# Kernel tuning notes

Hardware: AMD Instinct MI355X
Metric: run time of the kernel (lower is better)

## Reference

```python
import jax, jax.numpy as jnp
import numpy as np

N_NODES = 100000
N_EDGES = 1600000
B_GRAPHS = 64
F_IN = 128
HID = 128
N_CLS = 16
EPS = 1e-5


def setup_inputs() -> dict:
    key = jax.random.key(0)
    ks = jax.random.split(key, 12)
    x = jax.random.normal(ks[0], (N_NODES, F_IN), jnp.float32)
    edge_index = jax.random.randint(ks[1], (2, N_EDGES), 0, N_NODES, dtype=jnp.int32)
    batch = jnp.sort(jax.random.randint(ks[2], (N_NODES,), 0, B_GRAPHS, dtype=jnp.int32))
    sc = lambda fi: 1.0 / np.sqrt(fi)
    return {
        'x': x, 'edge_index': edge_index, 'batch': batch,
        'W1': jax.random.normal(ks[3], (F_IN, HID), jnp.float32) * sc(F_IN),
        'b1': jnp.zeros((HID,), jnp.float32),
        'g1': jnp.ones((HID,), jnp.float32), 'be1': jnp.zeros((HID,), jnp.float32),
        'W2': jax.random.normal(ks[4], (HID, HID), jnp.float32) * sc(HID),
        'b2': jnp.zeros((HID,), jnp.float32),
        'g2': jnp.ones((HID,), jnp.float32), 'be2': jnp.zeros((HID,), jnp.float32),
        'Wg1': jax.random.normal(ks[5], (HID, HID // 2), jnp.float32) * sc(HID),
        'bg1': jnp.zeros((HID // 2,), jnp.float32),
        'Wg2': jax.random.normal(ks[6], (HID // 2, 1), jnp.float32) * sc(HID // 2),
        'bg2': jnp.zeros((1,), jnp.float32),
        'Wc': jax.random.normal(ks[7], (HID, N_CLS), jnp.float32) * sc(HID),
        'bc': jnp.zeros((N_CLS,), jnp.float32),
    }


def gcn_conv(x, src, dst, W, b):
    # GCNConv: h = D^{-1/2}(A+I)D^{-1/2} (x W) + b, self-loops added
    n = x.shape[0]
    h = x @ W
    loop = jnp.arange(n, dtype=src.dtype)
    s = jnp.concatenate([src, loop])
    d = jnp.concatenate([dst, loop])
    deg = jax.ops.segment_sum(jnp.ones_like(d, dtype=h.dtype), d, num_segments=n)
    dinv = jax.lax.rsqrt(deg)  # deg >= 1 thanks to self-loops
    norm = dinv[s] * dinv[d]           # [E+N]
    msg = h[s] * norm[:, None]         # [E+N, HID] gather-transform
    return jax.ops.segment_sum(msg, d, num_segments=n) + b  # scatter-add


def layernorm(x, g, be):
    mu = jnp.mean(x, axis=-1, keepdims=True)
    var = jnp.mean(jnp.square(x - mu), axis=-1, keepdims=True)
    return (x - mu) * jax.lax.rsqrt(var + EPS) * g + be


def att_pool(x, batch, Wg1, bg1, Wg2, bg2, n_graphs):
    gate = jax.nn.relu(x @ Wg1 + bg1) @ Wg2 + bg2           # [N,1]
    gmax = jax.ops.segment_max(gate, batch, num_segments=n_graphs)
    e = jnp.exp(gate - gmax[batch])
    denom = jax.ops.segment_sum(e, batch, num_segments=n_graphs)
    alpha = e / denom[batch]                                 # segment softmax
    return jax.ops.segment_sum(alpha * x, batch, num_segments=n_graphs)


def reference(x, edge_index, batch, W1, b1, g1, be1, W2, b2, g2, be2,
              Wg1, bg1, Wg2, bg2, Wc, bc):
    src, dst = edge_index[0], edge_index[1]
    h = gcn_conv(x, src, dst, W1, b1)
    h = jax.nn.relu(layernorm(h, g1, be1))  # dropout is identity at eval
    h = gcn_conv(h, src, dst, W2, b2)
    h = jax.nn.relu(layernorm(h, g2, be2))
    pooled = att_pool(h, batch, Wg1, bg1, Wg2, bg2, B_GRAPHS)  # [B, HID]
    return pooled @ Wc + bc  # [B, N_CLS]
```

## Files before the change

kernel.cpp:

```cpp
#include <hip/hip_runtime.h>


typedef unsigned short ushort_t;
typedef unsigned int uint_t;
typedef __attribute__((ext_vector_type(8))) short short8;
typedef __attribute__((ext_vector_type(4))) float floatx4;

#define POOL_S 16
#define PAD_DEG 64

__device__ inline ushort_t bf16_rn(float f) {
  uint_t u = __float_as_uint(f);
  u += 0x7fffu + ((u >> 16) & 1u);
  return (ushort_t)(u >> 16);
}
__device__ inline float bf16_lo(uint_t v) { return __uint_as_float(v << 16); }
__device__ inline float bf16_hi(uint_t v) { return __uint_as_float(v & 0xffff0000u); }
__device__ inline uint_t bf16_pack(float a, float b) {
  return (uint_t)bf16_rn(a) | ((uint_t)bf16_rn(b) << 16);
}

__global__ __launch_bounds__(256) void prep_weights_kernel(
    const float* __restrict__ W1, const float* __restrict__ W2,
    const float* __restrict__ Wg1, ushort_t* __restrict__ Wt) {
  int id = blockIdx.x * 256 + threadIdx.x;
  float v;
  if (id < 16384) {
    int n = id >> 7, k = id & 127;
    v = W1[k * 128 + n];
  } else if (id < 32768) {
    int i2 = id - 16384;
    int n = i2 >> 7, k = i2 & 127;
    v = W2[k * 128 + n];
  } else {
    int i2 = id - 32768;
    int n = i2 >> 7, k = i2 & 127;
    v = Wg1[k * 64 + n];
  }
  Wt[id] = bf16_rn(v);
}

template <int TM, int NC, bool IN_F32, bool SCALE, bool BIASRELU, bool GATEDOT>
__device__ __forceinline__ void gemm_tile(
    const void* __restrict__ in, const ushort_t* __restrict__ Wt,
    const float* __restrict__ bias, const float* __restrict__ dinv,
    ushort_t* __restrict__ out, int M, int row0,
    const float* __restrict__ Wg2, const float* __restrict__ bg2,
    float* __restrict__ gate_out, short* As) {
  constexpr int CT = NC / 16;
  constexpr int RT = TM / 64;
  const int t = threadIdx.x;
#pragma unroll
  for (int i = 0; i < TM / 16; ++i) {
    int chunk = t + i * 256;
    int rr = chunk >> 4, c8 = (chunk & 15) * 8;
    int row = row0 + rr;
    short8 val = {0, 0, 0, 0, 0, 0, 0, 0};
    if (IN_F32) {
      const float* inf = (const float*)in;
      if (row < M) {
        float4 v0 = *(const float4*)(inf + (size_t)row * 128 + c8);
        float4 v1 = *(const float4*)(inf + (size_t)row * 128 + c8 + 4);
        val[0] = (short)bf16_rn(v0.x); val[1] = (short)bf16_rn(v0.y);
        val[2] = (short)bf16_rn(v0.z); val[3] = (short)bf16_rn(v0.w);
        val[4] = (short)bf16_rn(v1.x); val[5] = (short)bf16_rn(v1.y);
        val[6] = (short)bf16_rn(v1.z); val[7] = (short)bf16_rn(v1.w);
      }
    } else {
      const short* inb = (const short*)in;
      if (row < M) val = *(const short8*)(inb + (size_t)row * 128 + c8);
    }
    *(short8*)&As[rr * 136 + c8] = val;
  }
  __syncthreads();

  const int wave = t >> 6, lane = t & 63;
  const int m16 = lane & 15, quad = lane >> 4;
  floatx4 acc[RT][CT];
#pragma unroll
  for (int rt = 0; rt < RT; ++rt)
#pragma unroll
    for (int ct = 0; ct < CT; ++ct) acc[rt][ct] = (floatx4){0.f, 0.f, 0.f, 0.f};
#pragma unroll
  for (int ks = 0; ks < 4; ++ks) {
    int koff = ks * 32 + quad * 8;
    short8 a[RT];
#pragma unroll
    for (int rt = 0; rt < RT; ++rt)
      a[rt] = *(const short8*)&As[(wave * 16 + rt * 64 + m16) * 136 + koff];
#pragma unroll
    for (int ct = 0; ct < CT; ++ct) {
      short8 b = *(const short8*)((const short*)Wt + (size_t)(ct * 16 + m16) * 128 + koff);
#pragma unroll
      for (int rt = 0; rt < RT; ++rt)
        acc[rt][ct] = __builtin_amdgcn_mfma_f32_16x16x32_bf16(a[rt], b, acc[rt][ct], 0, 0, 0);
    }
  }

  float bv[CT];
  if (BIASRELU) {
#pragma unroll
    for (int ct = 0; ct < CT; ++ct) bv[ct] = bias[ct * 16 + m16];
  }

  if (GATEDOT) {
    float w2[CT];
#pragma unroll
    for (int ct = 0; ct < CT; ++ct) w2[ct] = Wg2[ct * 16 + m16];
    float bg2v = bg2[0];
#pragma unroll
    for (int rt = 0; rt < RT; ++rt) {
#pragma unroll
      for (int reg = 0; reg < 4; ++reg) {
        float p = 0.f;
#pragma unroll
        for (int ct = 0; ct < CT; ++ct)
          p += fmaxf(acc[rt][ct][reg] + bv[ct], 0.f) * w2[ct];
        p += __shfl_xor(p, 1);
        p += __shfl_xor(p, 2);
        p += __shfl_xor(p, 4);
        p += __shfl_xor(p, 8);
        if (m16 == 0) {
          int row = row0 + wave * 16 + rt * 64 + quad * 4 + reg;
          if (row < M) gate_out[row] = p + bg2v;
        }
      }
    }
    return;
  }

#pragma unroll
  for (int rt = 0; rt < RT; ++rt) {
#pragma unroll
    for (int reg = 0; reg < 4; ++reg) {
      int row = row0 + wave * 16 + rt * 64 + quad * 4 + reg;
      if (row < M) {
        float mult = SCALE ? dinv[row] : 1.f;
#pragma unroll
        for (int ct = 0; ct < CT; ++ct) {
          float v = acc[rt][ct][reg];
          if (BIASRELU) v = fmaxf(v + bv[ct], 0.f);
          else if (SCALE) v *= mult;
          out[(size_t)row * NC + ct * 16 + m16] = bf16_rn(v);
        }
      }
    }
  }
}

__global__ __launch_bounds__(256) void place_gemm1_kernel(
    const int* __restrict__ src, const int* __restrict__ dst,
    int* __restrict__ fill, int* __restrict__ srcs_pad, int E,
    const float* __restrict__ x, const ushort_t* __restrict__ Wt,
    ushort_t* __restrict__ hs, int M, int nPlace, int nGemm) {
  __shared__ short As[64 * 136];
  int b = blockIdx.x;
  int gi = b / 5, rem = b - gi * 5;
  if (rem == 4) {
    if (gi < nGemm)
      gemm_tile<64, 128, true, false, false, false>(
          x, Wt, nullptr, nullptr, hs, M, gi * 64, nullptr, nullptr, nullptr, As);
    return;
  }
  int pi = gi * 4 + rem;
  if (pi < nPlace) {
    int e = pi * 256 + threadIdx.x;
    if (e < E) {
      int d = dst[e];
      int pos = atomicAdd(&fill[d], 1);
      if (pos < PAD_DEG) srcs_pad[(size_t)d * PAD_DEG + pos] = src[e];
    }
  }
}

__global__ __launch_bounds__(256) void scale_dinv_kernel(
    uint4* __restrict__ hs4, const int* __restrict__ fill,
    float* __restrict__ dinv, int* __restrict__ srcs_pad,
    int Nnodes, int nU4) {
  int id = blockIdx.x * 256 + threadIdx.x;
  if (id >= nU4) return;
  int row = id >> 4;
  float dv = rsqrtf((float)(fill[row] + 1));
  uint4 v = hs4[id];
  uint4 o;
  o.x = bf16_pack(bf16_lo(v.x) * dv, bf16_hi(v.x) * dv);
  o.y = bf16_pack(bf16_lo(v.y) * dv, bf16_hi(v.y) * dv);
  o.z = bf16_pack(bf16_lo(v.z) * dv, bf16_hi(v.z) * dv);
  o.w = bf16_pack(bf16_lo(v.w) * dv, bf16_hi(v.w) * dv);
  hs4[id] = o;
  if ((id & 15) == 0) {
    dinv[row] = dv;
    int cnt = fill[row];
    if (cnt > PAD_DEG) cnt = PAD_DEG;
    int K = (cnt + 3) & ~3;
    for (int p = cnt; p < K; ++p) srcs_pad[(size_t)row * PAD_DEG + p] = Nnodes;
  }
}

template <int NC, bool SCALE, bool BIASRELU, bool GATEDOT>
__global__ __launch_bounds__(256) void gemm_mfma_kernel(
    const ushort_t* __restrict__ in, const ushort_t* __restrict__ Wt,
    const float* __restrict__ bias, const float* __restrict__ dinv,
    ushort_t* __restrict__ out, int M,
    const float* __restrict__ Wg2, const float* __restrict__ bg2,
    float* __restrict__ gate_out) {
  __shared__ short As[128 * 136];
  gemm_tile<128, NC, false, SCALE, BIASRELU, GATEDOT>(
      in, Wt, bias, dinv, out, M, blockIdx.x * 128, Wg2, bg2, gate_out, As);
}

__device__ __forceinline__ void add8(float* a, uint4 v) {
  a[0] += bf16_lo(v.x); a[1] += bf16_hi(v.x);
  a[2] += bf16_lo(v.y); a[3] += bf16_hi(v.y);
  a[4] += bf16_lo(v.z); a[5] += bf16_hi(v.z);
  a[6] += bf16_lo(v.w); a[7] += bf16_hi(v.w);
}

__global__ __launch_bounds__(256) void aggregate_ln_kernel(
    const ushort_t* __restrict__ hs, const int* __restrict__ fill,
    const int* __restrict__ srcs_pad, const float* __restrict__ dinv,
    const float* __restrict__ bias, const float* __restrict__ gamma,
    const float* __restrict__ beta, ushort_t* __restrict__ out, int N) {
  int n = (blockIdx.x * 256 + threadIdx.x) >> 6;
  int lane = threadIdx.x & 63;
  if (n >= N) return;
  const int col = lane & 15, epar = lane >> 4;
  const uint4* hs4 = (const uint4*)hs;
  int sreg = srcs_pad[(size_t)n * PAD_DEG + lane];
  int count = fill[n];
  if (count > PAD_DEG) count = PAD_DEG;
  const int K = (count + 3) & ~3;
  float a[8] = {0.f, 0.f, 0.f, 0.f, 0.f, 0.f, 0.f, 0.f};
  int i = epar;
  for (; i + 12 < K; i += 16) {
    int s0 = __shfl(sreg, i);
    int s1 = __shfl(sreg, i + 4);
    int s2 = __shfl(sreg, i + 8);
    int s3 = __shfl(sreg, i + 12);
    uint4 v0 = hs4[(size_t)s0 * 16 + col];
    uint4 v1 = hs4[(size_t)s1 * 16 + col];
    uint4 v2 = hs4[(size_t)s2 * 16 + col];
    uint4 v3 = hs4[(size_t)s3 * 16 + col];
    add8(a, v0); add8(a, v1); add8(a, v2); add8(a, v3);
  }
  for (; i < K; i += 4) {
    int s = __shfl(sreg, i);
    uint4 v = hs4[(size_t)s * 16 + col];
    add8(a, v);
  }
#pragma unroll
  for (int k = 0; k < 8; ++k) {
    a[k] += __shfl_xor(a[k], 16);
    a[k] += __shfl_xor(a[k], 32);
  }
  {
    uint4 sv = hs4[(size_t)n * 16 + col];
    add8(a, sv);
  }
  float dv = dinv[n];
  float4 b0 = *(const float4*)(bias + 8 * col);
  float4 b1 = *(const float4*)(bias + 8 * col + 4);
  float y[8];
  y[0] = a[0] * dv + b0.x; y[1] = a[1] * dv + b0.y;
  y[2] = a[2] * dv + b0.z; y[3] = a[3] * dv + b0.w;
  y[4] = a[4] * dv + b1.x; y[5] = a[5] * dv + b1.y;
  y[6] = a[6] * dv + b1.z; y[7] = a[7] * dv + b1.w;
  float s1 = 0.f, s2 = 0.f;
#pragma unroll
  for (int k = 0; k < 8; ++k) { s1 += y[k]; s2 += y[k] * y[k]; }
#pragma unroll
  for (int off = 1; off <= 8; off <<= 1) {
    s1 += __shfl_xor(s1, off);
    s2 += __shfl_xor(s2, off);
  }
  float mu = s1 * (1.f / 128.f);
  float var = s2 * (1.f / 128.f) - mu * mu;
  float rinv = rsqrtf(var + 1e-5f);
  float4 g0 = *(const float4*)(gamma + 8 * col);
  float4 g1 = *(const float4*)(gamma + 8 * col + 4);
  float4 e0 = *(const float4*)(beta + 8 * col);
  float4 e1 = *(const float4*)(beta + 8 * col + 4);
  float o[8];
  o[0] = fmaxf((y[0] - mu) * rinv * g0.x + e0.x, 0.f);
  o[1] = fmaxf((y[1] - mu) * rinv * g0.y + e0.y, 0.f);
  o[2] = fmaxf((y[2] - mu) * rinv * g0.z + e0.z, 0.f);
  o[3] = fmaxf((y[3] - mu) * rinv * g0.w + e0.w, 0.f);
  o[4] = fmaxf((y[4] - mu) * rinv * g1.x + e1.x, 0.f);
  o[5] = fmaxf((y[5] - mu) * rinv * g1.y + e1.y, 0.f);
  o[6] = fmaxf((y[6] - mu) * rinv * g1.z + e1.z, 0.f);
  o[7] = fmaxf((y[7] - mu) * rinv * g1.w + e1.w, 0.f);
  if (epar == 0) {
    uint4 pk;
    pk.x = bf16_pack(o[0], o[1]); pk.y = bf16_pack(o[2], o[3]);
    pk.z = bf16_pack(o[4], o[5]); pk.w = bf16_pack(o[6], o[7]);
    ((uint4*)out)[(size_t)n * 16 + col] = pk;
  }
}

__device__ inline int lower_bound_i(const int* a, int n, int key) {
  int lo = 0, hi = n;
  while (lo < hi) {
    int mid = (lo + hi) >> 1;
    if (a[mid] < key) lo = mid + 1; else hi = mid;
  }
  return lo;
}

__global__ __launch_bounds__(256) void gate_stats_kernel(
    const float* __restrict__ gate, const int* __restrict__ batch,
    float* __restrict__ gmax_out, float* __restrict__ ginv_out, int N) {
  int g = blockIdx.x, t = threadIdx.x;
  __shared__ float red[256];
  __shared__ float s_gmax;
  int lo = lower_bound_i(batch, N, g);
  int hi = lower_bound_i(batch, N, g + 1);
  float m = -3.4e38f;
  for (int i = lo + t; i < hi; i += 256) m = fmaxf(m, gate[i]);
  red[t] = m;
  __syncthreads();
  for (int off = 128; off; off >>= 1) {
    if (t < off) red[t] = fmaxf(red[t], red[t + off]);
    __syncthreads();
  }
  if (t == 0) s_gmax = red[0];
  __syncthreads();
  float gmax = s_gmax;
  __syncthreads();
  float ssum = 0.f;
  for (int i = lo + t; i < hi; i += 256) ssum += expf(gate[i] - gmax);
  red[t] = ssum;
  __syncthreads();
  for (int off = 128; off; off >>= 1) {
    if (t < off) red[t] += red[t + off];
    __syncthreads();
  }
  if (t == 0) {
    gmax_out[g] = gmax;
    ginv_out[g] = red[0] > 0.f ? 1.f / red[0] : 0.f;
  }
}

__global__ __launch_bounds__(256) void pool_partial_kernel(
    const ushort_t* __restrict__ h2, const float* __restrict__ gate,
    const int* __restrict__ batch, const float* __restrict__ gmax_in,
    float* __restrict__ partial, int N) {
  int g = blockIdx.x / POOL_S, sub = blockIdx.x % POOL_S;
  int t = threadIdx.x;
  __shared__ float redx[256];
  __shared__ float redy[256];
  int lo = lower_bound_i(batch, N, g);
  int hi = lower_bound_i(batch, N, g + 1);
  int len = hi - lo;
  int chunk = (len + POOL_S - 1) / POOL_S;
  int a = lo + sub * chunk;
  int b = a + chunk < hi ? a + chunk : hi;
  float gmax = gmax_in[g];
  int p = t & 63, strm = t >> 6;
  const uint_t* h2u = (const uint_t*)h2;
  float accx = 0.f, accy = 0.f;
  int i = a + strm;
  for (; i + 8 <= b; i += 8) {
    float e0 = expf(gate[i] - gmax);
    float e1 = expf(gate[i + 4] - gmax);
    uint_t v0 = h2u[(size_t)i * 64 + p];
    uint_t v1 = h2u[(size_t)(i + 4) * 64 + p];
    accx += e0 * bf16_lo(v0) + e1 * bf16_lo(v1);
    accy += e0 * bf16_hi(v0) + e1 * bf16_hi(v1);
  }
  for (; i < b; i += 4) {
    float e = expf(gate[i] - gmax);
    uint_t v = h2u[(size_t)i * 64 + p];
    accx += e * bf16_lo(v);
    accy += e * bf16_hi(v);
  }
  redx[t] = accx;
  redy[t] = accy;
  __syncthreads();
  if (t < 64) {
    float px = redx[t] + redx[t + 64] + redx[t + 128] + redx[t + 192];
    float py = redy[t] + redy[t + 64] + redy[t + 128] + redy[t + 192];
    float* dstp = partial + (size_t)blockIdx.x * 128;
    dstp[2 * t] = px;
    dstp[2 * t + 1] = py;
  }
}

__global__ __launch_bounds__(128) void classify_kernel(
    const float* __restrict__ partial, const float* __restrict__ ginv,
    const float* __restrict__ Wc, const float* __restrict__ bc,
    float* __restrict__ out) {
  int g = blockIdx.x, t = threadIdx.x;
  __shared__ float pooled[128];
  float s = 0.f;
#pragma unroll
  for (int k = 0; k < POOL_S; ++k)
    s += partial[((size_t)g * POOL_S + k) * 128 + t];
  pooled[t] = s * ginv[g];
  __syncthreads();
  if (t < 16) {
    float o = bc[t];
    for (int ff = 0; ff < 128; ++ff) o = fmaf(pooled[ff], Wc[ff * 16 + t], o);
    out[g * 16 + t] = o;
  }
}

extern "C" void kernel_launch(void* const* d_in, const int* in_sizes, int n_in,
                              void* d_out, int out_size, void* d_ws, size_t ws_size,
                              hipStream_t stream) {
  const float* x   = (const float*)d_in[0];
  const int*   ei  = (const int*)d_in[1];
  const int*   bat = (const int*)d_in[2];
  const float* W1  = (const float*)d_in[3];
  const float* b1  = (const float*)d_in[4];
  const float* g1  = (const float*)d_in[5];
  const float* be1 = (const float*)d_in[6];
  const float* W2  = (const float*)d_in[7];
  const float* b2  = (const float*)d_in[8];
  const float* g2  = (const float*)d_in[9];
  const float* be2 = (const float*)d_in[10];
  const float* Wg1 = (const float*)d_in[11];
  const float* bg1 = (const float*)d_in[12];
  const float* Wg2 = (const float*)d_in[13];
  const float* bg2 = (const float*)d_in[14];
  const float* Wc  = (const float*)d_in[15];
  const float* bc  = (const float*)d_in[16];

  const int N = in_sizes[0] / 128;
  const int E = in_sizes[1] / 2;
  const int B = out_size / 16;
  const int* src = ei;
  const int* dst = ei + E;

  const int Np = (N + 3) & ~3;

  int* fill      = (int*)d_ws;
  float* dinv    = (float*)(fill + Np);
  float* gatep   = dinv + Np;
  float* gmax    = gatep + Np;
  float* ginv    = gmax + B;
  float* ppart   = ginv + B;
  int* srcs_pad  = (int*)(ppart + (size_t)B * POOL_S * 128);
  ushort_t* Wt   = (ushort_t*)(srcs_pad + (size_t)N * PAD_DEG);
  ushort_t* hs   = Wt + 40960;
  ushort_t* h1   = hs + (size_t)128 * (N + 1);

  hipMemsetAsync(fill, 0, sizeof(int) * (size_t)Np, stream);
  hipMemsetAsync(hs + (size_t)128 * N, 0, 256, stream);

  const int Pb = (E + 255) / 256;
  const int Gb64 = (N + 63) / 64;
  const int Gg128 = (N + 127) / 128;
  const int nU4 = N * 16;

  prep_weights_kernel<<<160, 256, 0, stream>>>(W1, W2, Wg1, Wt);

  int nGroups = (Pb + 3) / 4;
  if (Gb64 > nGroups) nGroups = Gb64;
  place_gemm1_kernel<<<5 * nGroups, 256, 0, stream>>>(
      src, dst, fill, srcs_pad, E, x, Wt, hs, N, Pb, Gb64);

  scale_dinv_kernel<<<(nU4 + 255) / 256, 256, 0, stream>>>(
      (uint4*)hs, fill, dinv, srcs_pad, N, nU4);

  aggregate_ln_kernel<<<(N + 3) / 4, 256, 0, stream>>>(
      hs, fill, srcs_pad, dinv, b1, g1, be1, h1, N);
  gemm_mfma_kernel<128, true, false, false><<<Gg128, 256, 0, stream>>>(
      h1, Wt + 16384, nullptr, dinv, hs, N, nullptr, nullptr, nullptr);
  aggregate_ln_kernel<<<(N + 3) / 4, 256, 0, stream>>>(
      hs, fill, srcs_pad, dinv, b2, g2, be2, h1, N);
  gemm_mfma_kernel<64, false, true, true><<<Gg128, 256, 0, stream>>>(
      h1, Wt + 32768, bg1, nullptr, nullptr, N, Wg2, bg2, gatep);

  gate_stats_kernel<<<B, 256, 0, stream>>>(gatep, bat, gmax, ginv, N);
  pool_partial_kernel<<<B * POOL_S, 256, 0, stream>>>(h1, gatep, bat, gmax, ppart, N);
  classify_kernel<<<B, 128, 0, stream>>>(ppart, ginv, Wc, bc, (float*)d_out);
}
```

Before: 414.5 us.

## Vectorize edge placement 8-per-thread and fuse gate stats into pooling via online softmax

The edge-placement part of the fused place/GEMM1 kernel now has each thread load 8 src/dst pairs with int4 loads and issue 8 independent atomics. The block interleave changes from 4 place blocks per GEMM block to 1 place block per 2 GEMM blocks. The separate gate_stats kernel is removed: each pool block computes a local max and exp-sum over its chunk, and classify_kernel merges the partials with a rescaled (online) softmax. This saves one launch and one pass over the gate array, at the cost of redundant reductions inside each pool block and more atomics in flight per thread.

Result: slower. 426.9 us (+3.0%).

```diff
diff --git a/kernel.cpp b/kernel.cpp
--- a/kernel.cpp
+++ b/kernel.cpp
@@ -155,20 +155,46 @@
     ushort_t* __restrict__ hs, int M, int nPlace, int nGemm) {
   __shared__ short As[64 * 136];
   int b = blockIdx.x;
-  int gi = b / 5, rem = b - gi * 5;
-  if (rem == 4) {
-    if (gi < nGemm)
+  int gi = b / 3, rem = b - gi * 3;
+  if (rem < 2) {
+    int g = gi * 2 + rem;
+    if (g < nGemm)
       gemm_tile<64, 128, true, false, false, false>(
-          x, Wt, nullptr, nullptr, hs, M, gi * 64, nullptr, nullptr, nullptr, As);
+          x, Wt, nullptr, nullptr, hs, M, g * 64, nullptr, nullptr, nullptr, As);
     return;
   }
-  int pi = gi * 4 + rem;
-  if (pi < nPlace) {
-    int e = pi * 256 + threadIdx.x;
-    if (e < E) {
-      int d = dst[e];
-      int pos = atomicAdd(&fill[d], 1);
-      if (pos < PAD_DEG) srcs_pad[(size_t)d * PAD_DEG + pos] = src[e];
+  if (gi < nPlace) {
+    int e0 = (gi * 256 + threadIdx.x) * 8;
+    if (e0 + 7 < E) {
+      int4 dA = *(const int4*)(dst + e0);
+      int4 dB = *(const int4*)(dst + e0 + 4);
+      int4 sA = *(const int4*)(src + e0);
+      int4 sB = *(const int4*)(src + e0 + 4);
+      int p0 = atomicAdd(&fill[dA.x], 1);
+      int p1 = atomicAdd(&fill[dA.y], 1);
+      int p2 = atomicAdd(&fill[dA.z], 1);
+      int p3 = atomicAdd(&fill[dA.w], 1);
+      int p4 = atomicAdd(&fill[dB.x], 1);
+      int p5 = atomicAdd(&fill[dB.y], 1);
+      int p6 = atomicAdd(&fill[dB.z], 1);
+      int p7 = atomicAdd(&fill[dB.w], 1);
+      if (p0 < PAD_DEG) srcs_pad[(size_t)dA.x * PAD_DEG + p0] = sA.x;
+      if (p1 < PAD_DEG) srcs_pad[(size_t)dA.y * PAD_DEG + p1] = sA.y;
+      if (p2 < PAD_DEG) srcs_pad[(size_t)dA.z * PAD_DEG + p2] = sA.z;
+      if (p3 < PAD_DEG) srcs_pad[(size_t)dA.w * PAD_DEG + p3] = sA.w;
+      if (p4 < PAD_DEG) srcs_pad[(size_t)dB.x * PAD_DEG + p4] = sB.x;
+      if (p5 < PAD_DEG) srcs_pad[(size_t)dB.y * PAD_DEG + p5] = sB.y;
+      if (p6 < PAD_DEG) srcs_pad[(size_t)dB.z * PAD_DEG + p6] = sB.z;
+      if (p7 < PAD_DEG) srcs_pad[(size_t)dB.w * PAD_DEG + p7] = sB.w;
+    } else {
+      for (int j = 0; j < 8; ++j) {
+        int e = e0 + j;
+        if (e < E) {
+          int d = dst[e];
+          int pos = atomicAdd(&fill[d], 1);
+          if (pos < PAD_DEG) srcs_pad[(size_t)d * PAD_DEG + pos] = src[e];
+        }
+      }
     }
   }
 }
@@ -306,55 +332,43 @@
   return lo;
 }
 
-__global__ __launch_bounds__(256) void gate_stats_kernel(
-    const float* __restrict__ gate, const int* __restrict__ batch,
-    float* __restrict__ gmax_out, float* __restrict__ ginv_out, int N) {
-  int g = blockIdx.x, t = threadIdx.x;
-  __shared__ float red[256];
-  __shared__ float s_gmax;
-  int lo = lower_bound_i(batch, N, g);
-  int hi = lower_bound_i(batch, N, g + 1);
-  float m = -3.4e38f;
-  for (int i = lo + t; i < hi; i += 256) m = fmaxf(m, gate[i]);
-  red[t] = m;
-  __syncthreads();
-  for (int off = 128; off; off >>= 1) {
-    if (t < off) red[t] = fmaxf(red[t], red[t + off]);
-    __syncthreads();
-  }
-  if (t == 0) s_gmax = red[0];
-  __syncthreads();
-  float gmax = s_gmax;
-  __syncthreads();
-  float ssum = 0.f;
-  for (int i = lo + t; i < hi; i += 256) ssum += expf(gate[i] - gmax);
-  red[t] = ssum;
-  __syncthreads();
-  for (int off = 128; off; off >>= 1) {
-    if (t < off) red[t] += red[t + off];
-    __syncthreads();
-  }
-  if (t == 0) {
-    gmax_out[g] = gmax;
-    ginv_out[g] = red[0] > 0.f ? 1.f / red[0] : 0.f;
-  }
-}
-
 __global__ __launch_bounds__(256) void pool_partial_kernel(
     const ushort_t* __restrict__ h2, const float* __restrict__ gate,
-    const int* __restrict__ batch, const float* __restrict__ gmax_in,
-    float* __restrict__ partial, int N) {
+    const int* __restrict__ batch, float* __restrict__ partial,
+    float2* __restrict__ pstat, int N) {
   int g = blockIdx.x / POOL_S, sub = blockIdx.x % POOL_S;
   int t = threadIdx.x;
   __shared__ float redx[256];
   __shared__ float redy[256];
+  __shared__ float s_m;
   int lo = lower_bound_i(batch, N, g);
   int hi = lower_bound_i(batch, N, g + 1);
   int len = hi - lo;
   int chunk = (len + POOL_S - 1) / POOL_S;
   int a = lo + sub * chunk;
   int b = a + chunk < hi ? a + chunk : hi;
-  float gmax = gmax_in[g];
+  float m = -3.4e38f;
+  for (int i = a + t; i < b; i += 256) m = fmaxf(m, gate[i]);
+  redx[t] = m;
+  __syncthreads();
+  for (int off = 128; off; off >>= 1) {
+    if (t < off) redx[t] = fmaxf(redx[t], redx[t + off]);
+    __syncthreads();
+  }
+  if (t == 0) s_m = redx[0];
+  __syncthreads();
+  float gmax = s_m;
+  __syncthreads();
+  float ssum = 0.f;
+  for (int i = a + t; i < b; i += 256) ssum += expf(gate[i] - gmax);
+  redx[t] = ssum;
+  __syncthreads();
+  for (int off = 128; off; off >>= 1) {
+    if (t < off) redx[t] += redx[t + off];
+    __syncthreads();
+  }
+  float denom = redx[0];
+  __syncthreads();
   int p = t & 63, strm = t >> 6;
   const uint_t* h2u = (const uint_t*)h2;
   float accx = 0.f, accy = 0.f;
@@ -383,19 +397,41 @@
     dstp[2 * t] = px;
     dstp[2 * t + 1] = py;
   }
+  if (t == 0) pstat[blockIdx.x] = make_float2(gmax, denom);
 }
 
 __global__ __launch_bounds__(128) void classify_kernel(
-    const float* __restrict__ partial, const float* __restrict__ ginv,
+    const float* __restrict__ partial, const float2* __restrict__ pstat,
     const float* __restrict__ Wc, const float* __restrict__ bc,
     float* __restrict__ out) {
   int g = blockIdx.x, t = threadIdx.x;
   __shared__ float pooled[128];
+  __shared__ float wgt[POOL_S];
+  __shared__ float s_inv;
+  if (t == 0) {
+    float M = -3.4e38f;
+    float2 st[POOL_S];
+#pragma unroll
+    for (int k = 0; k < POOL_S; ++k) {
+      st[k] = pstat[g * POOL_S + k];
+      M = fmaxf(M, st[k].x);
+    }
+    float total = 0.f;
+#pragma unroll
+    for (int k = 0; k < POOL_S; ++k) {
+      float w = expf(st[k].x - M);
+      wgt[k] = w;
+      total += st[k].y * w;
+    }
+    s_inv = total > 0.f ? 1.f / total : 0.f;
+  }
+  __syncthreads();
+  float inv = s_inv;
   float s = 0.f;
 #pragma unroll
   for (int k = 0; k < POOL_S; ++k)
-    s += partial[((size_t)g * POOL_S + k) * 128 + t];
-  pooled[t] = s * ginv[g];
+    s += partial[((size_t)g * POOL_S + k) * 128 + t] * wgt[k];
+  pooled[t] = s * inv;
   __syncthreads();
   if (t < 16) {
     float o = bc[t];
@@ -436,9 +472,8 @@
   int* fill      = (int*)d_ws;
   float* dinv    = (float*)(fill + Np);
   float* gatep   = dinv + Np;
-  float* gmax    = gatep + Np;
-  float* ginv    = gmax + B;
-  float* ppart   = ginv + B;
+  float2* pstat  = (float2*)(gatep + Np);
+  float* ppart   = (float*)(pstat + B * POOL_S);
   int* srcs_pad  = (int*)(ppart + (size_t)B * POOL_S * 128);
   ushort_t* Wt   = (ushort_t*)(srcs_pad + (size_t)N * PAD_DEG);
   ushort_t* hs   = Wt + 40960;
@@ -447,17 +482,18 @@
   hipMemsetAsync(fill, 0, sizeof(int) * (size_t)Np, stream);
   hipMemsetAsync(hs + (size_t)128 * N, 0, 256, stream);
 
-  const int Pb = (E + 255) / 256;
+  const int Pb8 = (E + 2047) / 2048;
   const int Gb64 = (N + 63) / 64;
   const int Gg128 = (N + 127) / 128;
   const int nU4 = N * 16;
 
   prep_weights_kernel<<<160, 256, 0, stream>>>(W1, W2, Wg1, Wt);
 
-  int nGroups = (Pb + 3) / 4;
-  if (Gb64 > nGroups) nGroups = Gb64;
-  place_gemm1_kernel<<<5 * nGroups, 256, 0, stream>>>(
-      src, dst, fill, srcs_pad, E, x, Wt, hs, N, Pb, Gb64);
+  int nTriples = Pb8;
+  int gemmTriples = (Gb64 + 1) / 2;
+  if (gemmTriples > nTriples) nTriples = gemmTriples;
+  place_gemm1_kernel<<<3 * nTriples, 256, 0, stream>>>(
+      src, dst, fill, srcs_pad, E, x, Wt, hs, N, Pb8, Gb64);
 
   scale_dinv_kernel<<<(nU4 + 255) / 256, 256, 0, stream>>>(
       (uint4*)hs, fill, dinv, srcs_pad, N, nU4);
@@ -471,7 +507,7 @@
   gemm_mfma_kernel<64, false, true, true><<<Gg128, 256, 0, stream>>>(
       h1, Wt + 32768, bg1, nullptr, nullptr, N, Wg2, bg2, gatep);
 
-  gate_stats_kernel<<<B, 256, 0, stream>>>(gatep, bat, gmax, ginv, N);
-  pool_partial_kernel<<<B * POOL_S, 256, 0, stream>>>(h1, gatep, bat, gmax, ppart, N);
-  classify_kernel<<<B, 128, 0, stream>>>(ppart, ginv, Wc, bc, (float*)d_out);
-}
+  pool_partial_kernel<<<B * POOL_S, 256, 0, stream>>>(
+      h1, gatep, bat, ppart, pstat, N);
+  classify_kernel<<<B, 128, 0, stream>>>(ppart, pstat, Wc, bc, (float*)d_out);
+}
```
